# Optimization experiments

Hardware: AMD Instinct MI355X
Metric: run time of the kernel (lower is better)

Reference implementation:

```python
import jax, jax.numpy as jnp
import numpy as np

B, T, C = 16, 512, 768
MULT = 4
D_IN = C * MULT          # 3072
HIDDEN = 1024
N_DATES = 16
STACK_SIZE, STACK_STRIDE = 4, 2
MAX_F = 512
N_MASK_TYPES = 5
N_SESSIONS = 4
SCALE = HIDDEN ** 0.5


def setup_inputs() -> dict:
    key = jax.random.key(0)
    ks = jax.random.split(key, 12)
    inp = {
        "spikes": jax.random.normal(ks[0], (B, T, C), dtype=jnp.float32),
        "spikes_mask": jnp.ones((B, T), dtype=jnp.int64),
        "spikes_timestamp": jax.random.randint(ks[1], (B, T), 0, 255).astype(jnp.int64),
        "date_idx": jax.random.randint(ks[2], (B,), 0, N_DATES).astype(jnp.int64),
        "mask_idx": 1,
        "session_idx": 3,
        # params
        "W_embed": jax.random.normal(ks[3], (N_DATES, D_IN, C), dtype=jnp.float32) * 0.02,
        "b_embed": jax.random.normal(ks[4], (N_DATES, D_IN), dtype=jnp.float32) * 0.02,
        "W_stack": jax.random.normal(ks[5], (HIDDEN, D_IN * STACK_SIZE), dtype=jnp.float32) * 0.02,
        "b_stack": jax.random.normal(ks[6], (HIDDEN,), dtype=jnp.float32) * 0.02,
        "pos_table": jax.random.normal(ks[7], (MAX_F, HIDDEN), dtype=jnp.float32) * 0.02,
        "prompt_table": jax.random.normal(ks[8], (N_MASK_TYPES, HIDDEN), dtype=jnp.float32) * 0.02,
        "session_table": jax.random.normal(ks[9], (N_SESSIONS, HIDDEN), dtype=jnp.float32) * 0.02,
    }
    return inp


def reference(spikes, spikes_mask, spikes_timestamp, date_idx, mask_idx, session_idx,
              W_embed, b_embed, W_stack, b_stack, pos_table, prompt_table, session_table):
    Bb = spikes.shape[0]
    # adapt branch: per-sample expert Linear, done as one gather + batched GEMM
    W = W_embed[date_idx]                      # [B, D_IN, C]
    b = b_embed[date_idx]                      # [B, D_IN]
    x = jnp.einsum('btc,bdc->btd', spikes, W) + b[:, None, :]   # [B, T, D_IN]
    x = jax.nn.gelu(x, approximate=False) * SCALE
    # unfold-based stacking: sliding windows over time
    L = (T - STACK_SIZE) // STACK_STRIDE + 1   # 255
    starts = jnp.arange(L) * STACK_STRIDE
    widx = starts[:, None] + jnp.arange(STACK_SIZE)             # [L, size]
    win = x[:, widx, :]                                         # [B, L, size, D_IN]
    stacked = win.reshape(Bb, L, STACK_SIZE * D_IN)
    x = stacked @ W_stack.T + b_stack                           # [B, L, HIDDEN]
    ts = spikes_timestamp[:, :L]
    mask = jnp.prod(spikes_mask[:, widx], axis=-1)              # [B, L]
    # positional embedding
    x = x + pos_table[ts]
    # prompt token
    x = jnp.concatenate(
        [jnp.broadcast_to(prompt_table[mask_idx][None, None, :], (Bb, 1, HIDDEN)), x], axis=1)
    mask = jnp.pad(mask, ((0, 0), (1, 0)), constant_values=1)
    ts = jnp.concatenate([jnp.zeros((Bb, 1), ts.dtype), ts + 1], axis=1)
    # session token
    x = jnp.concatenate(
        [jnp.broadcast_to(session_table[session_idx][None, None, :], (Bb, 1, HIDDEN)), x], axis=1)
    mask = jnp.pad(mask, ((0, 0), (1, 0)), constant_values=1)
    ts = jnp.concatenate([jnp.zeros((Bb, 1), ts.dtype), ts + 1], axis=1)
    # dropout is identity in eval
    return x, mask, ts
```

## Files before the change

### kernel.cpp

```cpp
#include <hip/hip_runtime.h>
#include <hip/hip_bf16.h>

#define BATCH   16
#define TT      512
#define CC      768
#define D_IN    3072
#define HIDDEN  1024
#define LL      255
#define OUTROWS 257
#define KSTACK  12288
#define N_DATES 16

typedef float f32x4 __attribute__((ext_vector_type(4)));
typedef __bf16 bf16x8 __attribute__((ext_vector_type(8)));
typedef unsigned short u16;

__device__ __forceinline__ u16 f2bf(float f) {
    unsigned u = __builtin_bit_cast(unsigned, f);
    u = (u + 0x7FFFu + ((u >> 16) & 1u)) >> 16;
    return (u16)u;
}

__device__ __forceinline__ bf16x8 lds_read8(const u16* p) {
    return __builtin_bit_cast(bf16x8, *(const uint4*)p);
}

__device__ __forceinline__ void gload16(const u16* g, u16* l) {
    __builtin_amdgcn_global_load_lds(
        (const __attribute__((address_space(1))) void*)g,
        (__attribute__((address_space(3))) void*)l, 16, 0, 0);
}

#define RING_PHASE(PH, S, CA, CB, NA, NB)                                          \
    {                                                                              \
        const int ph_ = (PH);                                                      \
        if (ph_ + 1 < (S)) {                                                       \
            if (ph_ + 2 < (S)) { asm volatile("s_waitcnt vmcnt(4)" ::: "memory"); }\
            else               { asm volatile("s_waitcnt vmcnt(0)" ::: "memory"); }\
            __builtin_amdgcn_s_barrier();                                          \
            const u16* Ab_ = Asm[(ph_ + 1) & 3];                                   \
            const u16* Bb_ = Bsm[(ph_ + 1) & 3];                                   \
            _Pragma("unroll")                                                      \
            for (int i_ = 0; i_ < 8; ++i_)                                         \
                NA[i_] = lds_read8(&Ab_[(wm * 64 + i_ * 8 + urow) * 64 + cfrag]);  \
            _Pragma("unroll")                                                      \
            for (int j_ = 0; j_ < 4; ++j_)                                         \
                NB[j_] = lds_read8(&Bb_[(wn * 32 + j_ * 8 + urow) * 64 + cfrag]);  \
            if (ph_ + 3 < (S)) STAGE(ph_ + 3);                                     \
        }                                                                          \
        __builtin_amdgcn_s_setprio(1);                                             \
        _Pragma("unroll")                                                          \
        for (int i_ = 0; i_ < 8; ++i_)                                             \
            _Pragma("unroll")                                                      \
            for (int j_ = 0; j_ < 4; ++j_)                                         \
                acc[i_][j_] = __builtin_amdgcn_mfma_f32_16x16x32_bf16(             \
                    CA[i_], CB[j_], acc[i_][j_], 0, 0, 0);                         \
        __builtin_amdgcn_s_setprio(0);                                             \
    }

__global__ __launch_bounds__(256) void cvt_wstack(const float* __restrict__ W, u16* __restrict__ out) {
    size_t i = ((size_t)blockIdx.x * 256 + threadIdx.x) * 4;
    size_t stride = (size_t)gridDim.x * 256 * 4;
    for (; i < (size_t)HIDDEN * KSTACK; i += stride) {
        float4 v = *(const float4*)(W + i);
        ushort4 o = make_ushort4(f2bf(v.x), f2bf(v.y), f2bf(v.z), f2bf(v.w));
        *(ushort4*)(out + i) = o;
    }
}

__global__ __launch_bounds__(256) void cvt_spikes(const float* __restrict__ in, u16* __restrict__ out) {
    size_t i = ((size_t)blockIdx.x * 256 + threadIdx.x) * 4;
    size_t stride = (size_t)gridDim.x * 256 * 4;
    for (; i < (size_t)BATCH * TT * CC; i += stride) {
        float4 v = *(const float4*)(in + i);
        ushort4 o = make_ushort4(f2bf(v.x), f2bf(v.y), f2bf(v.z), f2bf(v.w));
        *(ushort4*)(out + i) = o;
    }
}

__global__ __launch_bounds__(64) void date_flags(const int* __restrict__ date_idx, int* __restrict__ flags) {
    const int tid = threadIdx.x;
    if (tid < N_DATES) flags[tid] = 0;
    __syncthreads();
    if (tid < BATCH) flags[date_idx[tid]] = 1;
}

__global__ __launch_bounds__(256) void cvt_wembed(const float* __restrict__ W,
                                                  const int* __restrict__ flags,
                                                  u16* __restrict__ out) {
    const int date = blockIdx.y;
    if (!flags[date]) return;
    const size_t bofs = (size_t)date * D_IN * CC;
    const size_t i = bofs + ((size_t)blockIdx.x * 256 + threadIdx.x) * 4;
    float4 v = *(const float4*)(W + i);
    ushort4 o = make_ushort4(f2bf(v.x), f2bf(v.y), f2bf(v.z), f2bf(v.w));
    *(ushort4*)(out + i) = o;
}

__global__ __launch_bounds__(512, 2) void gemm1_bf(const u16* __restrict__ spk,
                                                   const u16* __restrict__ wemb,
                                                   const float* __restrict__ b_embed,
                                                   const int* __restrict__ date_idx,
                                                   u16* __restrict__ x1) {
    const int m0 = blockIdx.x * 256;
    const int n0 = blockIdx.y * 256;
    const int bb = blockIdx.z;
    const int date = date_idx[bb];
    const u16* A  = spk  + (size_t)bb   * TT * CC;
    const u16* Bw = wemb + (size_t)date * D_IN * CC;
    const int S = CC / 32;

    __shared__ u16 Asm[4][128 * 64];
    __shared__ u16 Bsm[4][128 * 64];

    const int tid  = threadIdx.x;
    const int lane = tid & 63;
    const int wave = tid >> 6;
    const int wm = wave >> 2;
    const int wn = wave & 3;

    const int lrow  = lane >> 3;
    const int scol  = ((lane & 7) ^ lrow) << 3;
    const int chalf = scol >> 5;
    const int gk    = scol & 31;

    f32x4 acc[8][4] = {};

    auto STAGE = [&](int slice) {
        const int slot = slice & 3;
        const int k0 = slice * 32;
        u16* Ad = Asm[slot];
        u16* Bd = Bsm[slot];
        #pragma unroll
        for (int p = 0; p < 2; ++p) {
            const int rbase = (wave + 8 * p) * 8;
            const int tr = 2 * (rbase + lrow) + chalf;
            gload16(A  + (size_t)(m0 + tr) * CC + k0 + gk, Ad + rbase * 64);
            gload16(Bw + (size_t)(n0 + tr) * CC + k0 + gk, Bd + rbase * 64);
        }
    };

    const int krow  = lane & 15;
    const int kcol  = (lane >> 4) << 3;
    const int cfrag = (kcol + ((krow & 1) << 5)) ^ ((krow >> 1) << 3);
    const int urow  = krow >> 1;

    bf16x8 afA[8], bfA[4], afB[8], bfB[4];

    STAGE(0); STAGE(1); STAGE(2);
    asm volatile("s_waitcnt vmcnt(8)" ::: "memory");
    __builtin_amdgcn_s_barrier();
    {
        const u16* Ab_ = Asm[0];
        const u16* Bb_ = Bsm[0];
        #pragma unroll
        for (int i = 0; i < 8; ++i)
            afA[i] = lds_read8(&Ab_[(wm * 64 + i * 8 + urow) * 64 + cfrag]);
        #pragma unroll
        for (int j = 0; j < 4; ++j)
            bfA[j] = lds_read8(&Bb_[(wn * 32 + j * 8 + urow) * 64 + cfrag]);
    }

    for (int t = 0; t < S; t += 2) {
        RING_PHASE(t,     S, afA, bfA, afB, bfB);
        RING_PHASE(t + 1, S, afB, bfB, afA, bfA);
    }

    const float* be = b_embed + (size_t)date * D_IN;
    #pragma unroll
    for (int i = 0; i < 8; ++i) {
        #pragma unroll
        for (int j = 0; j < 4; ++j) {
            const int col  = n0 + wn * 64 + j * 16 + (lane & 15);
            const float bias = be[col];
            const int rbase = m0 + wm * 128 + i * 16 + ((lane >> 4) << 2);
            #pragma unroll
            for (int q = 0; q < 4; ++q) {
                float v = acc[i][j][q] + bias;
                float g = 0.5f * v * (1.0f + erff(v * 0.70710678118654752f)) * 32.0f;
                x1[(size_t)bb * TT * D_IN + (size_t)(rbase + q) * D_IN + col] = f2bf(g);
            }
        }
    }
}

__global__ __launch_bounds__(256) void gemm1_f32(const float* __restrict__ spikes,
                                                 const float* __restrict__ W_embed,
                                                 const float* __restrict__ b_embed,
                                                 const int* __restrict__ date_idx,
                                                 u16* __restrict__ x1) {
    const int m0 = blockIdx.x * 128;
    const int n0 = blockIdx.y * 128;
    const int bb = blockIdx.z;
    const int date = date_idx[bb];
    const float* A  = spikes  + (size_t)bb  * TT * CC;
    const float* Bw = W_embed + (size_t)date * D_IN * CC;

    __shared__ u16 As[128 * 64];
    __shared__ u16 Bs[128 * 64];

    const int tid  = threadIdx.x;
    const int lane = tid & 63;
    const int wave = tid >> 6;
    const int wm = wave >> 1, wn = wave & 1;

    f32x4 acc[4][4] = {};

    for (int k0 = 0; k0 < CC; k0 += 64) {
        {
            const int c4 = tid & 15;
            int r = tid >> 4;
            #pragma unroll
            for (int p = 0; p < 8; ++p, r += 16) {
                float4 va = *(const float4*)(A  + (size_t)(m0 + r) * CC + k0 + c4 * 4);
                float4 vb = *(const float4*)(Bw + (size_t)(n0 + r) * CC + k0 + c4 * 4);
                const int col = c4 * 4;
                const int idx = r * 64 + (col ^ ((r & 7) << 3));
                *(ushort4*)(&As[idx]) = make_ushort4(f2bf(va.x), f2bf(va.y), f2bf(va.z), f2bf(va.w));
                *(ushort4*)(&Bs[idx]) = make_ushort4(f2bf(vb.x), f2bf(vb.y), f2bf(vb.z), f2bf(vb.w));
            }
        }
        __syncthreads();
        #pragma unroll
        for (int kk = 0; kk < 64; kk += 32) {
            bf16x8 af[4], bfr[4];
            const int krow = lane & 15;
            const int kcol = kk + ((lane >> 4) << 3);
            #pragma unroll
            for (int i = 0; i < 4; ++i) {
                const int ra = wm * 64 + i * 16 + krow;
                af[i]  = lds_read8(&As[ra * 64 + (kcol ^ ((ra & 7) << 3))]);
                const int rb = wn * 64 + i * 16 + krow;
                bfr[i] = lds_read8(&Bs[rb * 64 + (kcol ^ ((rb & 7) << 3))]);
            }
            #pragma unroll
            for (int i = 0; i < 4; ++i)
                #pragma unroll
                for (int j = 0; j < 4; ++j)
                    acc[i][j] = __builtin_amdgcn_mfma_f32_16x16x32_bf16(af[i], bfr[j], acc[i][j], 0, 0, 0);
        }
        __syncthreads();
    }

    const float* be = b_embed + (size_t)date * D_IN;
    #pragma unroll
    for (int i = 0; i < 4; ++i) {
        #pragma unroll
        for (int j = 0; j < 4; ++j) {
            const int col  = n0 + wn * 64 + j * 16 + (lane & 15);
            const float bias = be[col];
            const int rbase = m0 + wm * 64 + i * 16 + ((lane >> 4) << 2);
            #pragma unroll
            for (int q = 0; q < 4; ++q) {
                float v = acc[i][j][q] + bias;
                float g = 0.5f * v * (1.0f + erff(v * 0.70710678118654752f)) * 32.0f;
                x1[(size_t)bb * TT * D_IN + (size_t)(rbase + q) * D_IN + col] = f2bf(g);
            }
        }
    }
}

template <bool WRITE_PART>
__global__ __launch_bounds__(512, 2) void gemm2(const u16* __restrict__ x1,
                                                const u16* __restrict__ Wbf,
                                                float* __restrict__ part,
                                                const float* __restrict__ b_stack,
                                                const float* __restrict__ pos_table,
                                                const int* __restrict__ tstamp,
                                                float* __restrict__ out,
                                                int KS) {
    const int n0 = blockIdx.x * 256;
    const int ks = blockIdx.y;
    const int bb = blockIdx.z;
    const int KCH  = KSTACK / KS;
    const int kbeg = ks * KCH;
    const int S    = KCH / 32;
    const u16* Xb = x1 + (size_t)bb * TT * D_IN;

    __shared__ u16 Asm[4][128 * 64];
    __shared__ u16 Bsm[4][128 * 64];

    const int tid  = threadIdx.x;
    const int lane = tid & 63;
    const int wave = tid >> 6;
    const int wm = wave >> 2;
    const int wn = wave & 3;

    const int lrow  = lane >> 3;
    const int scol  = ((lane & 7) ^ lrow) << 3;
    const int chalf = scol >> 5;
    const int gk    = scol & 31;

    f32x4 acc[8][4] = {};

    auto STAGE = [&](int slice) {
        const int slot = slice & 3;
        const int k0 = kbeg + slice * 32;
        const int s  = k0 / D_IN;
        const int d0 = k0 % D_IN;
        u16* Ad = Asm[slot];
        u16* Bd = Bsm[slot];
        #pragma unroll
        for (int p = 0; p < 2; ++p) {
            const int rbase = (wave + 8 * p) * 8;
            const int tr = 2 * (rbase + lrow) + chalf;
            gload16(Xb + (size_t)(2 * tr + s) * D_IN + d0 + gk, Ad + rbase * 64);
            gload16(Wbf + (size_t)(n0 + tr) * KSTACK + k0 + gk, Bd + rbase * 64);
        }
    };

    const int krow  = lane & 15;
    const int kcol  = (lane >> 4) << 3;
    const int cfrag = (kcol + ((krow & 1) << 5)) ^ ((krow >> 1) << 3);
    const int urow  = krow >> 1;

    bf16x8 afA[8], bfA[4], afB[8], bfB[4];

    STAGE(0); STAGE(1); STAGE(2);
    asm volatile("s_waitcnt vmcnt(8)" ::: "memory");
    __builtin_amdgcn_s_barrier();
    {
        const u16* Ab_ = Asm[0];
        const u16* Bb_ = Bsm[0];
        #pragma unroll
        for (int i = 0; i < 8; ++i)
            afA[i] = lds_read8(&Ab_[(wm * 64 + i * 8 + urow) * 64 + cfrag]);
        #pragma unroll
        for (int j = 0; j < 4; ++j)
            bfA[j] = lds_read8(&Bb_[(wn * 32 + j * 8 + urow) * 64 + cfrag]);
    }

    for (int t = 0; t < S; t += 2) {
        RING_PHASE(t,     S, afA, bfA, afB, bfB);
        RING_PHASE(t + 1, S, afB, bfB, afA, bfA);
    }

    if (WRITE_PART) {
        float* pt = part + ((size_t)(ks * BATCH + bb) * 256) * HIDDEN;
        #pragma unroll
        for (int i = 0; i < 8; ++i) {
            #pragma unroll
            for (int j = 0; j < 4; ++j) {
                const int col = n0 + wn * 64 + j * 16 + (lane & 15);
                const int rb  = wm * 128 + i * 16 + ((lane >> 4) << 2);
                #pragma unroll
                for (int q = 0; q < 4; ++q)
                    pt[(size_t)(rb + q) * HIDDEN + col] = acc[i][j][q];
            }
        }
    } else {
        #pragma unroll
        for (int i = 0; i < 8; ++i) {
            #pragma unroll
            for (int j = 0; j < 4; ++j) {
                const int col = n0 + wn * 64 + j * 16 + (lane & 15);
                const int lb  = wm * 128 + i * 16 + ((lane >> 4) << 2);
                #pragma unroll
                for (int q = 0; q < 4; ++q) {
                    const int l = lb + q;
                    if (l < LL) {
                        const int tsv = tstamp[bb * TT + l];
                        float v = acc[i][j][q] + b_stack[col] + pos_table[(size_t)tsv * HIDDEN + col];
                        out[(size_t)bb * OUTROWS * HIDDEN + (size_t)(2 + l) * HIDDEN + col] = v;
                    }
                }
            }
        }
    }
}

__global__ __launch_bounds__(256) void reduce_ep(const float* __restrict__ part,
                                                 const float* __restrict__ b_stack,
                                                 const float* __restrict__ pos_table,
                                                 const int* __restrict__ tstamp,
                                                 float* __restrict__ out,
                                                 int KS) {
    const int idx = blockIdx.x * 256 + threadIdx.x;
    const int c4  = idx & (HIDDEN / 4 - 1);
    const int r   = idx >> 8;
    if (r >= BATCH * LL) return;
    const int l  = r % LL;
    const int bb = r / LL;
    float4 v = make_float4(0.f, 0.f, 0.f, 0.f);
    for (int ks = 0; ks < KS; ++ks) {
        float4 p = *(const float4*)(part + ((size_t)(ks * BATCH + bb) * 256 + l) * HIDDEN + c4 * 4);
        v.x += p.x; v.y += p.y; v.z += p.z; v.w += p.w;
    }
    const int tsv = tstamp[bb * TT + l];
    float4 bs = *(const float4*)(b_stack + c4 * 4);
    float4 ps = *(const float4*)(pos_table + (size_t)tsv * HIDDEN + c4 * 4);
    v.x += bs.x + ps.x; v.y += bs.y + ps.y; v.z += bs.z + ps.z; v.w += bs.w + ps.w;
    *(float4*)(out + ((size_t)bb * OUTROWS + 2 + l) * HIDDEN + c4 * 4) = v;
}

__global__ __launch_bounds__(256) void epilogue_misc(const int* __restrict__ smask,
                                                     const int* __restrict__ tstamp,
                                                     const int* __restrict__ mask_idx_p,
                                                     const int* __restrict__ session_idx_p,
                                                     const float* __restrict__ prompt_table,
                                                     const float* __restrict__ session_table,
                                                     float* __restrict__ out) {
    const int bb = blockIdx.x;
    const int tid = threadIdx.x;
    const int mi = mask_idx_p[0];
    const int si = session_idx_p[0];
    float* xb = out + (size_t)bb * OUTROWS * HIDDEN;
    for (int i = tid; i < HIDDEN; i += 256) {
        xb[i]          = session_table[(size_t)si * HIDDEN + i];
        xb[HIDDEN + i] = prompt_table[(size_t)mi * HIDDEN + i];
    }
    float* maskout = out + (size_t)BATCH * OUTROWS * HIDDEN + (size_t)bb * OUTROWS;
    float* tsout   = out + (size_t)BATCH * OUTROWS * HIDDEN + (size_t)BATCH * OUTROWS + (size_t)bb * OUTROWS;
    for (int j = tid; j < OUTROWS; j += 256) {
        if (j == 0)      { maskout[0] = 1.0f; tsout[0] = 0.0f; }
        else if (j == 1) { maskout[1] = 1.0f; tsout[1] = 1.0f; }
        else {
            const int l = j - 2;
            int m = 1;
            #pragma unroll
            for (int s = 0; s < 4; ++s) m *= smask[bb * TT + 2 * l + s];
            maskout[j] = (float)m;
            tsout[j]   = (float)(tstamp[bb * TT + l] + 2);
        }
    }
}

extern "C" void kernel_launch(void* const* d_in, const int* in_sizes, int n_in,
                              void* d_out, int out_size, void* d_ws, size_t ws_size,
                              hipStream_t stream) {
    const float* spikes      = (const float*)d_in[0];
    const int*   spikes_mask = (const int*)d_in[1];
    const int*   tstamp      = (const int*)d_in[2];
    const int*   date_idx    = (const int*)d_in[3];
    const int*   mask_idx    = (const int*)d_in[4];
    const int*   session_idx = (const int*)d_in[5];
    const float* W_embed     = (const float*)d_in[6];
    const float* b_embed     = (const float*)d_in[7];
    const float* W_stack     = (const float*)d_in[8];
    const float* b_stack     = (const float*)d_in[9];
    const float* pos_table   = (const float*)d_in[10];
    const float* prompt_tab  = (const float*)d_in[11];
    const float* session_tab = (const float*)d_in[12];
    float* out = (float*)d_out;

    const size_t X1_B   = (size_t)BATCH * TT * D_IN * 2;
    const size_t WBF_B  = (size_t)HIDDEN * KSTACK * 2;
    const size_t PART_B = (size_t)BATCH * 256 * HIDDEN * 4;
    const size_t FLAGS_B = 4096;
    const size_t SPK_B  = (size_t)BATCH * TT * CC * 2;
    const size_t WEMB_B = (size_t)N_DATES * D_IN * CC * 2;
    const size_t BASE   = X1_B + WBF_B;
    const size_t UNION_BF = FLAGS_B + SPK_B + WEMB_B;

    u16*   x1    = (u16*)d_ws;
    u16*   Wbf   = (u16*)((char*)d_ws + X1_B);
    int*   flags = (int*)((char*)d_ws + BASE);
    u16*   spkbf = (u16*)((char*)d_ws + BASE + FLAGS_B);
    u16*   wembf = (u16*)((char*)d_ws + BASE + FLAGS_B + SPK_B);
    float* part  = (float*)((char*)d_ws + BASE);

    const bool use_bf = (ws_size >= BASE + UNION_BF);
    int KS = 0;
    if (use_bf) KS = 4;
    else {
        size_t rem = (ws_size > BASE) ? (ws_size - BASE) : 0;
        KS = (int)(rem / PART_B); if (KS > 4) KS = 4;
    }

    cvt_wstack<<<2048, 256, 0, stream>>>(W_stack, Wbf);

    if (use_bf) {
        date_flags<<<1, 64, 0, stream>>>(date_idx, flags);
        cvt_spikes<<<2048, 256, 0, stream>>>(spikes, spkbf);
        cvt_wembed<<<dim3(D_IN * CC / 4 / 256, N_DATES), 256, 0, stream>>>(W_embed, flags, wembf);
        gemm1_bf<<<dim3(TT / 256, D_IN / 256, BATCH), 512, 0, stream>>>(spkbf, wembf, b_embed, date_idx, x1);
    } else {
        gemm1_f32<<<dim3(TT / 128, D_IN / 128, BATCH), 256, 0, stream>>>(spikes, W_embed, b_embed, date_idx, x1);
    }

    if (KS > 0) {
        gemm2<true><<<dim3(HIDDEN / 256, KS, BATCH), 512, 0, stream>>>(x1, Wbf, part, b_stack, pos_table, tstamp, out, KS);
        reduce_ep<<<(BATCH * LL * (HIDDEN / 4) + 255) / 256, 256, 0, stream>>>(part, b_stack, pos_table, tstamp, out, KS);
    } else {
        gemm2<false><<<dim3(HIDDEN / 256, 1, BATCH), 512, 0, stream>>>(x1, Wbf, part, b_stack, pos_table, tstamp, out, 1);
    }
    epilogue_misc<<<BATCH, 256, 0, stream>>>(spikes_mask, tstamp, mask_idx, session_idx,
                                             prompt_tab, session_tab, out);
}
```

Before: 255.7 us.

## Replace register double-buffered ring with two-phase per-slice LDS/MFMA schedule

```diff
diff --git a/kernel.cpp b/kernel.cpp
--- a/kernel.cpp
+++ b/kernel.cpp
@@ -30,33 +30,6 @@
         (const __attribute__((address_space(1))) void*)g,
         (__attribute__((address_space(3))) void*)l, 16, 0, 0);
 }
-
-#define RING_PHASE(PH, S, CA, CB, NA, NB)                                          \
-    {                                                                              \
-        const int ph_ = (PH);                                                      \
-        if (ph_ + 1 < (S)) {                                                       \
-            if (ph_ + 2 < (S)) { asm volatile("s_waitcnt vmcnt(4)" ::: "memory"); }\
-            else               { asm volatile("s_waitcnt vmcnt(0)" ::: "memory"); }\
-            __builtin_amdgcn_s_barrier();                                          \
-            const u16* Ab_ = Asm[(ph_ + 1) & 3];                                   \
-            const u16* Bb_ = Bsm[(ph_ + 1) & 3];                                   \
-            _Pragma("unroll")                                                      \
-            for (int i_ = 0; i_ < 8; ++i_)                                         \
-                NA[i_] = lds_read8(&Ab_[(wm * 64 + i_ * 8 + urow) * 64 + cfrag]);  \
-            _Pragma("unroll")                                                      \
-            for (int j_ = 0; j_ < 4; ++j_)                                         \
-                NB[j_] = lds_read8(&Bb_[(wn * 32 + j_ * 8 + urow) * 64 + cfrag]);  \
-            if (ph_ + 3 < (S)) STAGE(ph_ + 3);                                     \
-        }                                                                          \
-        __builtin_amdgcn_s_setprio(1);                                             \
-        _Pragma("unroll")                                                          \
-        for (int i_ = 0; i_ < 8; ++i_)                                             \
-            _Pragma("unroll")                                                      \
-            for (int j_ = 0; j_ < 4; ++j_)                                         \
-                acc[i_][j_] = __builtin_amdgcn_mfma_f32_16x16x32_bf16(             \
-                    CA[i_], CB[j_], acc[i_][j_], 0, 0, 0);                         \
-        __builtin_amdgcn_s_setprio(0);                                             \
-    }
 
 __global__ __launch_bounds__(256) void cvt_wstack(const float* __restrict__ W, u16* __restrict__ out) {
     size_t i = ((size_t)blockIdx.x * 256 + threadIdx.x) * 4;
@@ -96,6 +69,55 @@
     ushort4 o = make_ushort4(f2bf(v.x), f2bf(v.y), f2bf(v.z), f2bf(v.w));
     *(ushort4*)(out + i) = o;
 }
+
+#define SLICE_PHASES(T, S)                                                          \
+    {                                                                               \
+        const int t_ = (T);                                                         \
+        const u16* Ab_ = Asm[t_ & 3];                                               \
+        const u16* Bb_ = Bsm[t_ & 3];                                               \
+        bf16x8 a_[4], b_[4];                                                        \
+                                                         \
+        _Pragma("unroll")                                                           \
+        for (int i_ = 0; i_ < 4; ++i_)                                              \
+            a_[i_] = lds_read8(&Ab_[(wm * 64 + i_ * 8 + urow) * 64 + cfrag]);       \
+        _Pragma("unroll")                                                           \
+        for (int j_ = 0; j_ < 4; ++j_)                                              \
+            b_[j_] = lds_read8(&Bb_[(wn * 32 + j_ * 8 + urow) * 64 + cfrag]);       \
+        if (t_ + 3 < (S)) STAGE(t_ + 3);                                            \
+        __builtin_amdgcn_s_barrier();                                               \
+        asm volatile("s_waitcnt lgkmcnt(0)" ::: "memory");                          \
+        __builtin_amdgcn_sched_barrier(0);                                          \
+        __builtin_amdgcn_s_setprio(1);                                              \
+        _Pragma("unroll")                                                           \
+        for (int i_ = 0; i_ < 4; ++i_)                                              \
+            _Pragma("unroll")                                                       \
+            for (int j_ = 0; j_ < 4; ++j_)                                          \
+                acc[i_][j_] = __builtin_amdgcn_mfma_f32_16x16x32_bf16(              \
+                    a_[i_], b_[j_], acc[i_][j_], 0, 0, 0);                          \
+        __builtin_amdgcn_s_setprio(0);                                              \
+        __builtin_amdgcn_s_barrier();                                               \
+                                                         \
+        _Pragma("unroll")                                                           \
+        for (int i_ = 0; i_ < 4; ++i_)                                              \
+            a_[i_] = lds_read8(&Ab_[(wm * 64 + (4 + i_) * 8 + urow) * 64 + cfrag]); \
+        if (t_ + 1 < (S)) {                                                         \
+            if      (t_ + 3 < (S)) { asm volatile("s_waitcnt vmcnt(8)" ::: "memory"); } \
+            else if (t_ + 2 < (S)) { asm volatile("s_waitcnt vmcnt(4)" ::: "memory"); } \
+            else                   { asm volatile("s_waitcnt vmcnt(0)" ::: "memory"); } \
+        }                                                                           \
+        __builtin_amdgcn_s_barrier();                                               \
+        asm volatile("s_waitcnt lgkmcnt(0)" ::: "memory");                          \
+        __builtin_amdgcn_sched_barrier(0);                                          \
+        __builtin_amdgcn_s_setprio(1);                                              \
+        _Pragma("unroll")                                                           \
+        for (int i_ = 0; i_ < 4; ++i_)                                              \
+            _Pragma("unroll")                                                       \
+            for (int j_ = 0; j_ < 4; ++j_)                                          \
+                acc[4 + i_][j_] = __builtin_amdgcn_mfma_f32_16x16x32_bf16(          \
+                    a_[i_], b_[j_], acc[4 + i_][j_], 0, 0, 0);                      \
+        __builtin_amdgcn_s_setprio(0);                                              \
+        __builtin_amdgcn_s_barrier();                                               \
+    }
 
 __global__ __launch_bounds__(512, 2) void gemm1_bf(const u16* __restrict__ spk,
                                                    const u16* __restrict__ wemb,
@@ -145,26 +167,11 @@
     const int cfrag = (kcol + ((krow & 1) << 5)) ^ ((krow >> 1) << 3);
     const int urow  = krow >> 1;
 
-    bf16x8 afA[8], bfA[4], afB[8], bfB[4];
-
     STAGE(0); STAGE(1); STAGE(2);
     asm volatile("s_waitcnt vmcnt(8)" ::: "memory");
     __builtin_amdgcn_s_barrier();
-    {
-        const u16* Ab_ = Asm[0];
-        const u16* Bb_ = Bsm[0];
-        #pragma unroll
-        for (int i = 0; i < 8; ++i)
-            afA[i] = lds_read8(&Ab_[(wm * 64 + i * 8 + urow) * 64 + cfrag]);
-        #pragma unroll
-        for (int j = 0; j < 4; ++j)
-            bfA[j] = lds_read8(&Bb_[(wn * 32 + j * 8 + urow) * 64 + cfrag]);
-    }
-
-    for (int t = 0; t < S; t += 2) {
-        RING_PHASE(t,     S, afA, bfA, afB, bfB);
-        RING_PHASE(t + 1, S, afB, bfB, afA, bfA);
-    }
+
+    for (int t = 0; t < S; ++t) SLICE_PHASES(t, S);
 
     const float* be = b_embed + (size_t)date * D_IN;
     #pragma unroll
@@ -314,26 +321,11 @@
     const int cfrag = (kcol + ((krow & 1) << 5)) ^ ((krow >> 1) << 3);
     const int urow  = krow >> 1;
 
-    bf16x8 afA[8], bfA[4], afB[8], bfB[4];
-
     STAGE(0); STAGE(1); STAGE(2);
     asm volatile("s_waitcnt vmcnt(8)" ::: "memory");
     __builtin_amdgcn_s_barrier();
-    {
-        const u16* Ab_ = Asm[0];
-        const u16* Bb_ = Bsm[0];
-        #pragma unroll
-        for (int i = 0; i < 8; ++i)
-            afA[i] = lds_read8(&Ab_[(wm * 64 + i * 8 + urow) * 64 + cfrag]);
-        #pragma unroll
-        for (int j = 0; j < 4; ++j)
-            bfA[j] = lds_read8(&Bb_[(wn * 32 + j * 8 + urow) * 64 + cfrag]);
-    }
-
-    for (int t = 0; t < S; t += 2) {
-        RING_PHASE(t,     S, afA, bfA, afB, bfB);
-        RING_PHASE(t + 1, S, afB, bfB, afA, bfA);
-    }
+
+    for (int t = 0; t < S; ++t) SLICE_PHASES(t, S);
 
     if (WRITE_PART) {
         float* pt = part + ((size_t)(ks * BATCH + bb) * 256) * HIDDEN;
```

Result: slower. 283.9 us (+11.0%).
